# Performance work log

Measured on AMD Instinct MI355X. Metric: run time of the kernel, lower is better.

Reference implementation:

```python
import jax, jax.numpy as jnp
from jax import lax
import numpy as np

RADIUS = 0.2
NSAMPLE = 64


def _ball_query(xyz, new_xyz, radius, nsample):
    """Faithful PointNet++ ball query.

    For each center, take the first `nsample` point indices (in index order)
    whose squared distance < radius^2; if fewer than nsample are found, the
    remaining slots are filled with the first found index (CUDA kernel
    semantics). Returns int32 idx of shape (B, npoint, nsample).
    """
    N = xyz.shape[1]
    # (B, npoint, N) squared distances
    d2 = jnp.sum((new_xyz[:, :, None, :] - xyz[:, None, :, :]) ** 2, axis=-1)
    within = d2 < (radius * radius)
    # key = point index if within ball, else N (sentinel); smallest nsample
    # keys == first nsample in-ball indices in index order.
    key = jnp.where(within, jnp.arange(N, dtype=jnp.int32), jnp.int32(N))
    neg_vals, _ = lax.top_k(-key, nsample)          # largest of -key = smallest key
    sel = -neg_vals                                  # (B, npoint, nsample)
    valid = sel < N
    first = jnp.where(valid[..., :1], sel[..., :1], 0)  # first found idx (or 0)
    return jnp.where(valid, sel, first)


def _group_gather(features, idx):
    # features: (B, C, N), idx: (B, npoint, nsample) -> (B, C, npoint, nsample)
    return jax.vmap(lambda f, i: f[:, i])(features, idx)


def setup_inputs() -> dict:
    key = jax.random.key(0)
    k1, k2, k3 = jax.random.split(key, 3)
    B, N, npoint, C = 4, 16384, 2048, 64
    xyz = jax.random.uniform(k1, (B, N, 3), dtype=jnp.float32)
    new_xyz = jax.random.uniform(k2, (B, npoint, 3), dtype=jnp.float32)
    features = jax.random.normal(k3, (B, C, N), dtype=jnp.float32)
    return {"xyz": xyz, "new_xyz": new_xyz, "features": features}


def reference(xyz, new_xyz, features):
    idx = _ball_query(xyz, new_xyz, RADIUS, NSAMPLE)          # (B, npoint, nsample)
    xyz_t = jnp.transpose(xyz, (0, 2, 1))                      # (B, 3, N)
    grouped_xyz = _group_gather(xyz_t, idx)                    # (B, 3, npoint, nsample)
    grouped_xyz = grouped_xyz - jnp.transpose(new_xyz, (0, 2, 1))[..., None]
    grouped_features = _group_gather(features, idx)            # (B, C, npoint, nsample)
    new_features = jnp.concatenate([grouped_xyz, grouped_features], axis=1)
    # original code does .transpose(1, 2) -> (B, npoint, 3+C, nsample)
    return jnp.transpose(new_features, (0, 2, 1, 3))
```

## Files before the change

kernel.cpp:

```cpp
#include <hip/hip_runtime.h>


#define BB 4
#define NN 16384
#define NP 2048
#define CC 64
#define NS 64
#define CH (3 + CC)
#define NCHUNK (NN / 256)

__global__ __launch_bounds__(256) void pn2_transpose_kernel(
    const float* __restrict__ f, float* __restrict__ ft)
{
    __shared__ float tile[CC][65];
    const int b   = blockIdx.x >> 8;
    const int n0  = (blockIdx.x & 255) << 6;
    const int col = threadIdx.x & 63;
    const int r4  = threadIdx.x >> 6;
    const float* src = f + (size_t)b * CC * NN;
#pragma unroll
    for (int i = 0; i < 16; ++i) {
        const int c = r4 + i * 4;
        tile[c][col] = __builtin_nontemporal_load(&src[(size_t)c * NN + n0 + col]);
    }
    __syncthreads();
    float* dst = ft + ((size_t)b * NN + n0) * CC;
#pragma unroll
    for (int i = 0; i < 16; ++i) {
        const int n = r4 + i * 4;
        dst[(size_t)n * CC + col] = tile[col][n];
    }
}

__global__ __launch_bounds__(256, 4) void pn2_qg_kernel(
    const float* __restrict__ xyz,
    const float* __restrict__ new_xyz,
    const float* __restrict__ ft,
    float* __restrict__ out)
{
    __shared__ int sidx[4][NS];
    __shared__ float4 stile[4][32 * 16];

    const int lane = threadIdx.x & 63;
    const int wave = threadIdx.x >> 6;
    const int center = blockIdx.x * 4 + wave;
    const int b = center >> 11;
    const int j = center & (NP - 1);

    const float r2 = 0.04f;
    const float* q = new_xyz + ((size_t)b * NP + j) * 3;
    const float cx = q[0], cy = q[1], cz = q[2];

    const float* xb = xyz + (size_t)b * NN * 3;
    const float4* x4 = (const float4*)xb;
    int* widx = sidx[wave];

    const int base = 3 * lane;
    const unsigned long long low = (1ull << lane) - 1ull;
    int found = 0;
    int it = 0;
    float4 A = x4[base], Bv = x4[base + 1], Cv = x4[base + 2];

    while (true) {
        const int nit = (it + 1 < NCHUNK) ? it + 1 : it;
        const size_t nb = (size_t)nit * 192 + base;
        float4 nA = x4[nb], nB = x4[nb + 1], nC = x4[nb + 2];

        const int n0 = it * 256 + 4 * lane;
        const float px[4] = {A.x, A.w, Bv.z, Cv.y};
        const float py[4] = {A.y, Bv.x, Bv.w, Cv.z};
        const float pz[4] = {A.z, Bv.y, Cv.x, Cv.w};
        bool in[4];
        unsigned long long m[4];
#pragma unroll
        for (int k = 0; k < 4; ++k) {
            const float dx = px[k] - cx;
            const float dy = py[k] - cy;
            const float dz = pz[k] - cz;
            const float d2 = __fadd_rn(__fadd_rn(__fmul_rn(dx, dx), __fmul_rn(dy, dy)),
                                       __fmul_rn(dz, dz));
            in[k] = d2 < r2;
            m[k] = __ballot(in[k]);
        }
        int pos = found
                + (int)__popcll(m[0] & low) + (int)__popcll(m[1] & low)
                + (int)__popcll(m[2] & low) + (int)__popcll(m[3] & low);
#pragma unroll
        for (int k = 0; k < 4; ++k) {
            if (in[k]) {
                if (pos < NS) widx[pos] = n0 + k;
                ++pos;
            }
        }
        found += (int)(__popcll(m[0]) + __popcll(m[1])
                     + __popcll(m[2]) + __popcll(m[3]));
        if (found >= NS || it == NCHUNK - 1) break;
        A = nA; Bv = nB; Cv = nC; ++it;
    }

    int myidx = 0;
    if (found > 0) {
        const int first = widx[0];
        myidx = (lane < found) ? widx[lane] : first;
    }
    widx[lane] = myidx;

    const float* pp = xb + (size_t)myidx * 3;
    float* ob = out + (size_t)center * CH * NS;
    __builtin_nontemporal_store(pp[0] - cx, ob + 0 * NS + lane);
    __builtin_nontemporal_store(pp[1] - cy, ob + 1 * NS + lane);
    __builtin_nontemporal_store(pp[2] - cz, ob + 2 * NS + lane);

    const float* ftb = ft + (size_t)b * NN * CC;
    float4* tw = stile[wave];
    const int sub  = lane & 15;
    const int rsub = lane >> 4;
    const int s_loc = lane & 31;
    const int which = lane >> 5;

#pragma unroll
    for (int h = 0; h < 2; ++h) {
        int ridx[8];
#pragma unroll
        for (int i = 0; i < 8; ++i) ridx[i] = widx[32 * h + 4 * i + rsub];
        float4 v[8];
#pragma unroll
        for (int i = 0; i < 8; ++i)
            v[i] = *(const float4*)(ftb + (size_t)ridx[i] * CC + 4 * sub);
#pragma unroll
        for (int i = 0; i < 8; ++i) {
            const int s = 4 * i + rsub;
            tw[s * 16 + (sub ^ (s & 15))] = v[i];
        }
#pragma unroll
        for (int t = 0; t < 8; ++t) {
            const int cq = 2 * t + which;
            const float4 u = tw[s_loc * 16 + (cq ^ (s_loc & 15))];
            float* o = ob + (size_t)(3 + 4 * cq) * NS + 32 * h + s_loc;
            __builtin_nontemporal_store(u.x, o + 0 * NS);
            __builtin_nontemporal_store(u.y, o + 1 * NS);
            __builtin_nontemporal_store(u.z, o + 2 * NS);
            __builtin_nontemporal_store(u.w, o + 3 * NS);
        }
    }
}

__global__ __launch_bounds__(256, 4) void pn2_group_kernel(
    const float* __restrict__ xyz, const float* __restrict__ new_xyz,
    const float* __restrict__ features, float* __restrict__ out)
{
    __shared__ int sidx[4][NS];
    const int lane = threadIdx.x & 63;
    const int wave = threadIdx.x >> 6;
    const int center = blockIdx.x * 4 + wave;
    const int b = center >> 11;
    const int j = center & (NP - 1);
    const float r2 = 0.04f;
    const float* q = new_xyz + ((size_t)b * NP + j) * 3;
    const float cx = q[0], cy = q[1], cz = q[2];
    int* widx = sidx[wave];
    int found = 0;
    for (int it = 0; it < NN / 64; ++it) {
        const int n = it * 64 + lane;
        const float* p = xyz + ((size_t)b * NN + n) * 3;
        const float dx = p[0] - cx, dy = p[1] - cy, dz = p[2] - cz;
        const float d2 = __fadd_rn(__fadd_rn(__fmul_rn(dx, dx), __fmul_rn(dy, dy)),
                                   __fmul_rn(dz, dz));
        const bool within = d2 < r2;
        const unsigned long long mask = __ballot(within);
        const int pos = found + (int)__popcll(mask & ((1ull << lane) - 1ull));
        if (within && pos < NS) widx[pos] = n;
        found += (int)__popcll(mask);
        if (found >= NS) break;
    }
    int myidx = 0;
    if (found > 0) {
        const int first = widx[0];
        myidx = (lane < found) ? widx[lane] : first;
    }
    const float* pp = xyz + ((size_t)b * NN + myidx) * 3;
    float* ob = out + (((size_t)b * NP + j) * (size_t)CH) * NS + lane;
    ob[0 * NS] = pp[0] - cx;
    ob[1 * NS] = pp[1] - cy;
    ob[2 * NS] = pp[2] - cz;
    const float* fb = features + (size_t)b * CC * NN + myidx;
#pragma unroll 8
    for (int c = 0; c < CC; ++c) ob[(size_t)(3 + c) * NS] = fb[(size_t)c * NN];
}

extern "C" void kernel_launch(void* const* d_in, const int* in_sizes, int n_in,
                              void* d_out, int out_size, void* d_ws, size_t ws_size,
                              hipStream_t stream) {
    const float* xyz      = (const float*)d_in[0];
    const float* new_xyz  = (const float*)d_in[1];
    const float* features = (const float*)d_in[2];
    float* out = (float*)d_out;

    const size_t ft_bytes = (size_t)BB * NN * CC * sizeof(float);

    if (ws_size >= ft_bytes) {
        float* ft = (float*)d_ws;
        pn2_transpose_kernel<<<BB * 256, 256, 0, stream>>>(features, ft);
        pn2_qg_kernel<<<BB * NP / 4, 256, 0, stream>>>(xyz, new_xyz, ft, out);
    } else {
        pn2_group_kernel<<<BB * NP / 4, 256, 0, stream>>>(xyz, new_xyz, features, out);
    }
}
```

Before: 49.25 us.

## Remap blocks per XCD by batch and vectorize output stores via padded LDS transpose

Block indices are remapped so each pair of XCDs handles one batch, keeping that batch's transposed features and xyz in a shared L2 instead of spreading every batch across all XCDs. The feature write-out also changes: the LDS tile is now a padded scalar layout (stride 65), so each lane gathers four consecutive samples and issues one 16-byte nontemporal store instead of four scalar stores. This trades more scalar LDS reads and writes for fewer, wider global stores and better L2 locality.

```diff
diff --git a/kernel.cpp b/kernel.cpp
--- a/kernel.cpp
+++ b/kernel.cpp
@@ -8,13 +8,19 @@
 #define NS 64
 #define CH (3 + CC)
 #define NCHUNK (NN / 256)
+#define ST 65
+
+typedef float f32x4 __attribute__((ext_vector_type(4)));
 
 __global__ __launch_bounds__(256) void pn2_transpose_kernel(
     const float* __restrict__ f, float* __restrict__ ft)
 {
     __shared__ float tile[CC][65];
-    const int b   = blockIdx.x >> 8;
-    const int n0  = (blockIdx.x & 255) << 6;
+    const int g = blockIdx.x;
+    const int xcd = g & 7;
+    const int b = xcd >> 1;
+    const int tidx = ((xcd & 1) << 7) + (g >> 3);
+    const int n0 = tidx << 6;
     const int col = threadIdx.x & 63;
     const int r4  = threadIdx.x >> 6;
     const float* src = f + (size_t)b * CC * NN;
@@ -39,11 +45,15 @@
     float* __restrict__ out)
 {
     __shared__ int sidx[4][NS];
-    __shared__ float4 stile[4][32 * 16];
+    __shared__ float stile[4][32 * ST];
 
     const int lane = threadIdx.x & 63;
     const int wave = threadIdx.x >> 6;
-    const int center = blockIdx.x * 4 + wave;
+
+    const int g = blockIdx.x;
+    const int xcd = g & 7;
+    const int cg = ((xcd >> 1) << 9) + ((xcd & 1) << 8) + (g >> 3);
+    const int center = cg * 4 + wave;
     const int b = center >> 11;
     const int j = center & (NP - 1);
 
@@ -112,11 +122,11 @@
     __builtin_nontemporal_store(pp[2] - cz, ob + 2 * NS + lane);
 
     const float* ftb = ft + (size_t)b * NN * CC;
-    float4* tw = stile[wave];
+    float* tw = stile[wave];
     const int sub  = lane & 15;
     const int rsub = lane >> 4;
-    const int s_loc = lane & 31;
-    const int which = lane >> 5;
+    const int sq   = lane & 7;
+    const int cc8  = lane >> 3;
 
 #pragma unroll
     for (int h = 0; h < 2; ++h) {
@@ -129,18 +139,19 @@
             v[i] = *(const float4*)(ftb + (size_t)ridx[i] * CC + 4 * sub);
 #pragma unroll
         for (int i = 0; i < 8; ++i) {
-            const int s = 4 * i + rsub;
-            tw[s * 16 + (sub ^ (s & 15))] = v[i];
+            float* tr = tw + (4 * i + rsub) * ST + 4 * sub;
+            tr[0] = v[i].x; tr[1] = v[i].y; tr[2] = v[i].z; tr[3] = v[i].w;
         }
 #pragma unroll
         for (int t = 0; t < 8; ++t) {
-            const int cq = 2 * t + which;
-            const float4 u = tw[s_loc * 16 + (cq ^ (s_loc & 15))];
-            float* o = ob + (size_t)(3 + 4 * cq) * NS + 32 * h + s_loc;
-            __builtin_nontemporal_store(u.x, o + 0 * NS);
-            __builtin_nontemporal_store(u.y, o + 1 * NS);
-            __builtin_nontemporal_store(u.z, o + 2 * NS);
-            __builtin_nontemporal_store(u.w, o + 3 * NS);
+            const int c = 8 * t + cc8;
+            f32x4 u;
+            u.x = tw[(4 * sq + 0) * ST + c];
+            u.y = tw[(4 * sq + 1) * ST + c];
+            u.z = tw[(4 * sq + 2) * ST + c];
+            u.w = tw[(4 * sq + 3) * ST + c];
+            float* o = ob + (size_t)(3 + c) * NS + 32 * h + 4 * sq;
+            __builtin_nontemporal_store(u, (f32x4*)o);
         }
     }
 }
```

Measured after the change: 46.09 us. 6.4% less time.
